# Optimization experiments

Hardware: AMD Instinct MI355X
Metric: run time of the kernel (lower is better)

Reference implementation:

```python
import jax, jax.numpy as jnp
import numpy as np

N = 96          # max_nodes
MPM_ITERS = 50  # fixed iteration count (early-stop tol check omitted for jit determinism)
EDGE_PROB = 0.05


def setup_inputs() -> dict:
    key = jax.random.key(0)
    k1, k2 = jax.random.split(key)
    # symmetric binary ground-truth adjacency with unit diagonal (self loops)
    u = jax.random.uniform(k1, (N, N))
    upper = jnp.triu((u < EDGE_PROB).astype(jnp.float32), 1)
    A_gt = upper + upper.T + jnp.eye(N, dtype=jnp.float32)
    # decoder output: upper-triangular (no diag) edge logits
    vec_logits = jax.random.normal(k2, (N * (N - 1) // 2,), dtype=jnp.float32)
    return {"A_gt": A_gt, "vec_logits": vec_logits}


def _vec_to_adj(vec, n):
    iu = jnp.triu_indices(n, 1)
    adj = jnp.zeros((n, n), vec.dtype).at[iu].set(vec)
    adj = adj + adj.T
    return adj.at[jnp.diag_indices(n)].set(1.0)


def _edge_sim_tensor(A, B, degA, degB):
    # S[i,j,a,b] = A[i,j]*A[i,i]*A[j,j]*B[a,b]*B[a,a]*B[b,b], with
    # (i==j) xor (a==b) zeroed, and the i==j,a==b diagonal replaced by the
    # node-similarity block dA[i]*dB[a]*deg_sim(degA[i],degB[a]).
    n = A.shape[0]
    node_sim = 1.0 / (jnp.abs(degA[:, None] - degB[None, :]) + 1.0)
    dA = jnp.diagonal(A)
    dB = jnp.diagonal(B)
    S = (A[:, :, None, None]
         * dA[:, None, None, None] * dA[None, :, None, None]
         * B[None, None, :, :]
         * dB[None, None, :, None] * dB[None, None, None, :])
    eye = jnp.eye(n, dtype=bool)
    zero_mask = eye[:, :, None, None] ^ eye[None, None, :, :]  # (i==j) xor (a==b)
    S = jnp.where(zero_mask, 0.0, S)
    idx = jnp.arange(n)
    ii = idx[:, None]
    aa = idx[None, :]
    node_block = dA[:, None] * dB[None, :] * node_sim
    S = S.at[ii, ii, aa, aa].set(node_block)
    return S


def _mpm(X0, S, iters=MPM_ITERS):
    n = X0.shape[0]
    idx = jnp.arange(n)
    node_sim = S[idx[:, None], idx[:, None], idx[None, :], idx[None, :]]  # (N,N)
    mask = (~jnp.eye(n, dtype=bool))[:, :, None].astype(S.dtype)          # (i,j,1)

    @jax.checkpoint
    def step(X, _):
        # XS_max[i,j,a] = max_b S[i,j,a,b] * X[j,b]
        XS_max = (S * X[None, :, None, :]).max(axis=-1)
        X_new = X * node_sim + (XS_max * mask).sum(axis=1)
        X_new = X_new / jnp.linalg.norm(X_new)
        return X_new, None

    X, _ = jax.lax.scan(step, X0, None, length=iters)
    return X


def reference(A_gt, vec_logits):
    n = A_gt.shape[0]
    A_hat_logits = _vec_to_adj(vec_logits, n)
    B = jax.nn.sigmoid(A_hat_logits)
    degA = A_gt.sum(axis=1)
    degB = jax.lax.stop_gradient(B).sum(axis=1)  # torch: .sigmoid().detach().sum(1)
    S = _edge_sim_tensor(A_gt, B, degA, degB)
    X0 = jnp.full((n, n), 1.0 / n, dtype=A_gt.dtype)
    return _mpm(X0, S)
```

## Files before the change

kernel.cpp:

```cpp
#include <hip/hip_runtime.h>
#include <math.h>

#define N 96
#define PAD 100
#define T 768
#define ITERS 50
#define LW 52

typedef float f2 __attribute__((ext_vector_type(2)));
typedef unsigned short u16x4 __attribute__((ext_vector_type(4)));

template <int CTRL>
__device__ __forceinline__ float dppmax(float m) {
    int mi = __builtin_bit_cast(int, m);
    int sw = __builtin_amdgcn_update_dpp(mi, mi, CTRL, 0xf, 0xf, true);
    return fmaxf(m, __builtin_bit_cast(float, sw));
}
#define DPP_XOR1 0xB1
#define DPP_XOR2 0x4E

__global__ __launch_bounds__(T)
__attribute__((amdgpu_waves_per_eu(3, 3)))
void k_fused(const float* __restrict__ A,
             const float* __restrict__ vec,
             float* __restrict__ out) {
    __shared__ float Xs[N * PAD];
    __shared__ float Ms[(N + 1) * PAD];
    __shared__ unsigned short lst[N * LW];
    __shared__ short cnt4[N];
    __shared__ float degA[N];
    __shared__ float degB[N];
    __shared__ float red[T / 64];

    const int t = threadIdx.x;
    const int q = t & 3;
    const int p = t >> 2;
    const int ap = p % 48;
    const int g = p / 48;
    const int a0 = 2 * ap;
    const int ac = t % 48;
    const int ri = t / 48;
    const float s1 = 1.0f / (1.0f + expf(-1.0f));
    const float s1s1 = s1 * s1;

#pragma unroll
    for (int k = 0; k < 12; ++k) {
        int e = t + k * T;
        int r = e / N, c = e % N;
        float logit;
        if (r == c) {
            logit = 1.0f;
        } else {
            int i = r < c ? r : c;
            int j = r < c ? c : r;
            int idx = i * 95 - (i * (i - 1)) / 2 + (j - i - 1);
            logit = vec[idx];
        }
        Xs[r * PAD + c] = 1.0f / (1.0f + expf(-logit));
    }
    __syncthreads();

    f2 Wp0[12], Wp1[12];
#pragma unroll
    for (int k = 0; k < 12; ++k) {
        int b = 24 * q + 2 * k;
        float w00 = Xs[b * PAD + a0] * s1s1;
        float w01 = Xs[(b + 1) * PAD + a0] * s1s1;
        float w10 = Xs[b * PAD + a0 + 1] * s1s1;
        float w11 = Xs[(b + 1) * PAD + a0 + 1] * s1s1;
        if (b == a0) w00 = 0.0f;
        if (b + 1 == a0) w01 = 0.0f;
        if (b == a0 + 1) w10 = 0.0f;
        if (b + 1 == a0 + 1) w11 = 0.0f;
        Wp0[k] = (f2){w00, w01};
        Wp1[k] = (f2){w10, w11};
    }

    if (t < N) {
        float s = 0.f;
        for (int r = 0; r < N; ++r) s += Xs[r * PAD + t];
        degB[t] = s;
    }
    __syncthreads();

#pragma unroll
    for (int k = 0; k < 12; ++k) {
        int e = t + k * T;
        Xs[(e / N) * PAD + (e % N)] = A[e];
    }
    __syncthreads();

    if (t < N) {
        float s = 0.f;
        for (int r = 0; r < N; ++r) s += Xs[r * PAD + t];
        degA[t] = s;
    } else if (t < 2 * N) {
        int i = t - N;
        int c_ = 0;
        for (int j = 0; j < N; ++j) {
            if (j != i && Xs[j * PAD + i] > 0.5f)
                lst[i * LW + c_++] = (unsigned short)(j * PAD * 4);
        }
        while (c_ & 3) lst[i * LW + c_++] = (unsigned short)(N * PAD * 4);
        cnt4[i] = (short)c_;
    }
    if (t < PAD) Ms[N * PAD + t] = 0.0f;
    __syncthreads();

    f2 ns2[6], x2[6];
#pragma unroll
    for (int k = 0; k < 6; ++k) {
        int i = ri + 16 * k;
        ns2[k] = (f2){s1 / (fabsf(degA[i] - degB[2 * ac]) + 1.0f),
                      s1 / (fabsf(degA[i] - degB[2 * ac + 1]) + 1.0f)};
        x2[k] = (f2){1.0f / 96.0f, 1.0f / 96.0f};
    }

#pragma unroll
    for (int k = 0; k < 12; ++k) {
        int e = t + k * T;
        Xs[(e / N) * PAD + (e % N)] = (1.0f / 96.0f);
    }
    __syncthreads();

    const float* xbase = &Xs[g * PAD + 24 * q];
    const char* MsaB = (const char*)Ms + 8 * ac;

    for (int it = 0; it < ITERS; ++it) {
#pragma unroll 6
        for (int jj = 0; jj < 24; ++jj) {
            const float* xr = xbase + jj * 4 * PAD;
            float m0 = 0.f, m1 = 0.f;
#pragma unroll
            for (int c = 0; c < 6; ++c) {
                float4 x = *(const float4*)(xr + 4 * c);
                f2 xA = (f2){x.x, x.y};
                f2 xB = (f2){x.z, x.w};
                f2 pa = Wp0[2 * c] * xA;
                f2 pb = Wp0[2 * c + 1] * xB;
                m0 = fmaxf(fmaxf(m0, pa.x), pa.y);
                m0 = fmaxf(fmaxf(m0, pb.x), pb.y);
                f2 qa = Wp1[2 * c] * xA;
                f2 qb = Wp1[2 * c + 1] * xB;
                m1 = fmaxf(fmaxf(m1, qa.x), qa.y);
                m1 = fmaxf(fmaxf(m1, qb.x), qb.y);
            }
            m0 = dppmax<DPP_XOR1>(m0);
            m0 = dppmax<DPP_XOR2>(m0);
            m1 = dppmax<DPP_XOR1>(m1);
            m1 = dppmax<DPP_XOR2>(m1);
            if (q == 0)
                *(float2*)&Ms[(4 * jj + g) * PAD + a0] = make_float2(m0, m1);
        }
        __syncthreads();

        f2 y2[6];
#pragma unroll
        for (int k = 0; k < 6; ++k) {
            int i = ri + 16 * k;
            f2 acc = x2[k] * ns2[k];
            int nch = (int)cnt4[i] >> 2;
            const unsigned short* lp = &lst[i * LW];
            for (int cc = 0; cc < nch; ++cc) {
                u16x4 o = *(const u16x4*)(lp + 4 * cc);
                acc += *(const f2*)(MsaB + o.x);
                acc += *(const f2*)(MsaB + o.y);
                acc += *(const f2*)(MsaB + o.z);
                acc += *(const f2*)(MsaB + o.w);
            }
            y2[k] = acc;
        }

        float ss = 0.f;
#pragma unroll
        for (int k = 0; k < 6; ++k) {
            ss = fmaf(y2[k].x, y2[k].x, ss);
            ss = fmaf(y2[k].y, y2[k].y, ss);
        }
#pragma unroll
        for (int mm = 1; mm < 64; mm <<= 1) ss += __shfl_xor(ss, mm, 64);
        if ((t & 63) == 0) red[t >> 6] = ss;
        __syncthreads();
        float s = 0.f;
#pragma unroll
        for (int w2 = 0; w2 < T / 64; ++w2) s += red[w2];
        float inv = 1.0f / sqrtf(s);
        f2 inv2 = (f2){inv, inv};
#pragma unroll
        for (int k = 0; k < 6; ++k) {
            int i = ri + 16 * k;
            f2 xn = y2[k] * inv2;
            x2[k] = xn;
            *(f2*)&Xs[i * PAD + 2 * ac] = xn;
        }
        __syncthreads();
    }

#pragma unroll
    for (int k = 0; k < 12; ++k) {
        int e = t + k * T;
        out[e] = Xs[(e / N) * PAD + (e % N)];
    }
}

extern "C" void kernel_launch(void* const* d_in, const int* in_sizes, int n_in,
                              void* d_out, int out_size, void* d_ws, size_t ws_size,
                              hipStream_t stream) {
    const float* A = (const float*)d_in[0];
    const float* vec = (const float*)d_in[1];
    float* out = (float*)d_out;
    k_fused<<<1, T, 0, stream>>>(A, vec, out);
}
```

Measured before the change: 594.0 us.

## Retile max-product loop so each thread covers six columns over twelve b values

The thread mapping for the XS_max stage changes. Each thread now owns six output columns and a 12-wide slice of b, with 8 lanes per column group and 6 row groups. Each X row slice loaded from LDS is reused across six weight columns, which cuts LDS reads per thread, and the max reductions use packed elementwise max. In exchange, register pressure rises (36 f2 weights) and cross-lane work grows, since there are more DPP reductions, now including a row_shl:4 step to combine eight lanes.

```diff
diff --git a/kernel.cpp b/kernel.cpp
--- a/kernel.cpp
+++ b/kernel.cpp
@@ -8,6 +8,7 @@
 #define LW 52
 
 typedef float f2 __attribute__((ext_vector_type(2)));
+typedef float f4 __attribute__((ext_vector_type(4)));
 typedef unsigned short u16x4 __attribute__((ext_vector_type(4)));
 
 template <int CTRL>
@@ -18,6 +19,7 @@
 }
 #define DPP_XOR1 0xB1
 #define DPP_XOR2 0x4E
+#define DPP_SHL4 0x104
 
 __global__ __launch_bounds__(T)
 __attribute__((amdgpu_waves_per_eu(3, 3)))
@@ -33,11 +35,10 @@
     __shared__ float red[T / 64];
 
     const int t = threadIdx.x;
-    const int q = t & 3;
-    const int p = t >> 2;
-    const int ap = p % 48;
-    const int g = p / 48;
-    const int a0 = 2 * ap;
+    const int g = t / 128;
+    const int r = t % 128;
+    const int q = r & 7;
+    const int cs = r >> 3;
     const int ac = t % 48;
     const int ri = t / 48;
     const float s1 = 1.0f / (1.0f + expf(-1.0f));
@@ -46,39 +47,36 @@
 #pragma unroll
     for (int k = 0; k < 12; ++k) {
         int e = t + k * T;
-        int r = e / N, c = e % N;
+        int rr = e / N, cc = e % N;
         float logit;
-        if (r == c) {
+        if (rr == cc) {
             logit = 1.0f;
         } else {
-            int i = r < c ? r : c;
-            int j = r < c ? c : r;
+            int i = rr < cc ? rr : cc;
+            int j = rr < cc ? cc : rr;
             int idx = i * 95 - (i * (i - 1)) / 2 + (j - i - 1);
             logit = vec[idx];
         }
-        Xs[r * PAD + c] = 1.0f / (1.0f + expf(-logit));
-    }
-    __syncthreads();
-
-    f2 Wp0[12], Wp1[12];
-#pragma unroll
-    for (int k = 0; k < 12; ++k) {
-        int b = 24 * q + 2 * k;
-        float w00 = Xs[b * PAD + a0] * s1s1;
-        float w01 = Xs[(b + 1) * PAD + a0] * s1s1;
-        float w10 = Xs[b * PAD + a0 + 1] * s1s1;
-        float w11 = Xs[(b + 1) * PAD + a0 + 1] * s1s1;
-        if (b == a0) w00 = 0.0f;
-        if (b + 1 == a0) w01 = 0.0f;
-        if (b == a0 + 1) w10 = 0.0f;
-        if (b + 1 == a0 + 1) w11 = 0.0f;
-        Wp0[k] = (f2){w00, w01};
-        Wp1[k] = (f2){w10, w11};
+        Xs[rr * PAD + cc] = 1.0f / (1.0f + expf(-logit));
+    }
+    __syncthreads();
+
+    f2 Wp[6][6];
+#pragma unroll
+    for (int c = 0; c < 6; ++c) {
+        int col = 6 * cs + c;
+#pragma unroll
+        for (int bp = 0; bp < 6; ++bp) {
+            int b = 12 * q + 2 * bp;
+            float w0 = (b == col) ? 0.f : Xs[b * PAD + col] * s1s1;
+            float w1 = (b + 1 == col) ? 0.f : Xs[(b + 1) * PAD + col] * s1s1;
+            Wp[c][bp] = (f2){w0, w1};
+        }
     }
 
     if (t < N) {
         float s = 0.f;
-        for (int r = 0; r < N; ++r) s += Xs[r * PAD + t];
+        for (int rr = 0; rr < N; ++rr) s += Xs[rr * PAD + t];
         degB[t] = s;
     }
     __syncthreads();
@@ -92,7 +90,7 @@
 
     if (t < N) {
         float s = 0.f;
-        for (int r = 0; r < N; ++r) s += Xs[r * PAD + t];
+        for (int rr = 0; rr < N; ++rr) s += Xs[rr * PAD + t];
         degA[t] = s;
     } else if (t < 2 * N) {
         int i = t - N;
@@ -123,34 +121,40 @@
     }
     __syncthreads();
 
-    const float* xbase = &Xs[g * PAD + 24 * q];
+    const float* xbase = &Xs[g * PAD + 12 * q];
     const char* MsaB = (const char*)Ms + 8 * ac;
 
     for (int it = 0; it < ITERS; ++it) {
-#pragma unroll 6
-        for (int jj = 0; jj < 24; ++jj) {
-            const float* xr = xbase + jj * 4 * PAD;
-            float m0 = 0.f, m1 = 0.f;
+#pragma unroll 4
+        for (int jj = 0; jj < 16; ++jj) {
+            const float* xr = xbase + jj * 6 * PAD;
+            f4 Xa = *(const f4*)(xr);
+            f4 Xb = *(const f4*)(xr + 4);
+            f4 Xc = *(const f4*)(xr + 8);
+            f2 xp0 = (f2){Xa.x, Xa.y}, xp1 = (f2){Xa.z, Xa.w};
+            f2 xp2 = (f2){Xb.x, Xb.y}, xp3 = (f2){Xb.z, Xb.w};
+            f2 xp4 = (f2){Xc.x, Xc.y}, xp5 = (f2){Xc.z, Xc.w};
+            float mc[6];
 #pragma unroll
             for (int c = 0; c < 6; ++c) {
-                float4 x = *(const float4*)(xr + 4 * c);
-                f2 xA = (f2){x.x, x.y};
-                f2 xB = (f2){x.z, x.w};
-                f2 pa = Wp0[2 * c] * xA;
-                f2 pb = Wp0[2 * c + 1] * xB;
-                m0 = fmaxf(fmaxf(m0, pa.x), pa.y);
-                m0 = fmaxf(fmaxf(m0, pb.x), pb.y);
-                f2 qa = Wp1[2 * c] * xA;
-                f2 qb = Wp1[2 * c + 1] * xB;
-                m1 = fmaxf(fmaxf(m1, qa.x), qa.y);
-                m1 = fmaxf(fmaxf(m1, qb.x), qb.y);
+                f2 p = Wp[c][0] * xp0;
+                p = __builtin_elementwise_max(p, Wp[c][1] * xp1);
+                p = __builtin_elementwise_max(p, Wp[c][2] * xp2);
+                p = __builtin_elementwise_max(p, Wp[c][3] * xp3);
+                p = __builtin_elementwise_max(p, Wp[c][4] * xp4);
+                p = __builtin_elementwise_max(p, Wp[c][5] * xp5);
+                float m = fmaxf(p.x, p.y);
+                m = dppmax<DPP_XOR1>(m);
+                m = dppmax<DPP_XOR2>(m);
+                m = dppmax<DPP_SHL4>(m);
+                mc[c] = m;
             }
-            m0 = dppmax<DPP_XOR1>(m0);
-            m0 = dppmax<DPP_XOR2>(m0);
-            m1 = dppmax<DPP_XOR1>(m1);
-            m1 = dppmax<DPP_XOR2>(m1);
-            if (q == 0)
-                *(float2*)&Ms[(4 * jj + g) * PAD + a0] = make_float2(m0, m1);
+            if (q == 0) {
+                float* dst = &Ms[(6 * jj + g) * PAD + 6 * cs];
+                *(f2*)(dst)     = (f2){mc[0], mc[1]};
+                *(f2*)(dst + 2) = (f2){mc[2], mc[3]};
+                *(f2*)(dst + 4) = (f2){mc[4], mc[5]};
+            }
         }
         __syncthreads();
 
```

New measurement: 745.3 us. 25.5% more time.
